# Performance work log

Measured on AMD Instinct MI355X. Metric: run time of the kernel, lower is better.

The kernel has to match this reference:

```python
import jax, jax.numpy as jnp
import numpy as np
import math

B, N, D = 2, 2048, 1024
H = 16
HD = D // H
WINDOW = 256
LN_EPS = 1e-5
NEG_INF = float('-inf')


def _alibi_slopes(num_heads):
    # num_heads=16 is a power of two -> no extra-slope branch
    closest = 2 ** math.floor(math.log2(num_heads))
    base = 2.0 ** (-(2.0 ** (-(math.log2(closest) - 3))))
    return np.power(base, np.arange(1, closest + 1, dtype=np.float32))


def setup_inputs() -> dict:
    key = jax.random.key(0)
    ks = jax.random.split(key, 8)
    s = 0.02
    return {
        'x': jax.random.normal(ks[0], (B, N, D), dtype=jnp.float32),
        'qkv_w': jax.random.normal(ks[1], (D, 3 * D), dtype=jnp.float32) * s,
        'qkv_b': jnp.zeros((3 * D,), jnp.float32),
        'proj_w': jax.random.normal(ks[2], (D, D), dtype=jnp.float32) * s,
        'proj_b': jnp.zeros((D,), jnp.float32),
        'ln1_g': jnp.ones((D,), jnp.float32),
        'ln1_b': jnp.zeros((D,), jnp.float32),
        'ln2_g': jnp.ones((D,), jnp.float32),
        'ln2_b': jnp.zeros((D,), jnp.float32),
        'fc1_w': jax.random.normal(ks[3], (D, 4 * D), dtype=jnp.float32) * s,
        'fc1_b': jnp.zeros((4 * D,), jnp.float32),
        'fc2_w': jax.random.normal(ks[4], (4 * D, D), dtype=jnp.float32) * s,
        'fc2_b': jnp.zeros((D,), jnp.float32),
    }


def _layernorm(x, g, b):
    mu = jnp.mean(x, axis=-1, keepdims=True)
    var = jnp.mean(jnp.square(x - mu), axis=-1, keepdims=True)
    return (x - mu) * jax.lax.rsqrt(var + LN_EPS) * g + b


def reference(x, qkv_w, qkv_b, proj_w, proj_b, ln1_g, ln1_b, ln2_g, ln2_b,
              fc1_w, fc1_b, fc2_w, fc2_b):
    # ---- ALiBi sliding-window causal attention (pre-norm) ----
    h = _layernorm(x, ln1_g, ln1_b)
    qkv = (h @ qkv_w + qkv_b).reshape(B, N, 3, H, HD)
    q, k, v = [jnp.transpose(qkv[:, :, i], (0, 2, 1, 3)) for i in range(3)]  # [B,H,N,HD]

    scale = HD ** -0.5
    attn = jnp.einsum('bhqd,bhkd->bhqk', q, k) * scale  # [B,H,N,N]

    pos = jnp.arange(N)
    rel = pos[None, :] - pos[:, None]                      # rel[i,j] = j - i
    slopes = jnp.asarray(_alibi_slopes(H))                 # [H]
    a = slopes[:, None, None] * jnp.abs(rel).astype(jnp.float32)
    alibi = jnp.where(rel < 0, -a, a)                      # == slopes * rel
    attn = attn + alibi[None]

    # sliding-window mask: +1.0 inside window (faithful to ones-init), -inf outside
    sw = jnp.where(jnp.abs(rel) >= WINDOW, NEG_INF, 1.0)
    attn = attn + sw[None, None]

    # causal mask
    attn = jnp.where((rel > 0)[None, None], NEG_INF, attn)

    p = jax.nn.softmax(attn, axis=-1)
    o = jnp.einsum('bhqk,bhkd->bhqd', p, v)
    o = jnp.transpose(o, (0, 2, 1, 3)).reshape(B, N, D)
    x = x + (o @ proj_w + proj_b)

    # ---- FFN (Linear -> exact GELU -> Linear), pre-norm residual ----
    h2 = _layernorm(x, ln2_g, ln2_b)
    ff = jax.nn.gelu(h2 @ fc1_w + fc1_b, approximate=False) @ fc2_w + fc2_b
    return x + ff
```

## Files before the change

kernel.cpp:

```cpp
#include <hip/hip_runtime.h>
#include <stdint.h>

typedef unsigned short u16;
typedef __attribute__((ext_vector_type(8))) short bf16x8;
typedef __attribute__((ext_vector_type(4))) float f32x4;

__device__ __forceinline__ u16 f2bf(float f) {
  union { float f; unsigned u; } x; x.f = f;
  unsigned r = x.u + 0x7fffu + ((x.u >> 16) & 1u);
  return (u16)(r >> 16);
}

__device__ __forceinline__ float gelu_fast(float v) {
  float y = 0.7978845608f * (v + 0.044715f * v * v * v);
  float e = __expf(2.0f * y);
  float th = 1.0f - 2.0f / (e + 1.0f);
  return 0.5f * v * (1.0f + th);
}

#define GLOAD16(g, l) __builtin_amdgcn_global_load_lds( \
    (const __attribute__((address_space(1))) unsigned int*)(g), \
    (__attribute__((address_space(3))) unsigned int*)(l), 16, 0, 0)

__global__ __launch_bounds__(256) void pre_kernel(
    const float* __restrict__ qkv_w, const float* __restrict__ proj_w,
    const float* __restrict__ fc1_w, const float* __restrict__ fc2_w,
    u16* __restrict__ qkvw_t, u16* __restrict__ projw_t,
    u16* __restrict__ fc1w_t, u16* __restrict__ fc2w_t,
    const float* __restrict__ x, const float* __restrict__ g,
    const float* __restrict__ be, u16* __restrict__ h1) {
  __shared__ float tile[32][33];
  __shared__ float p1[4], p2[4];
  const int bid = blockIdx.x, t = threadIdx.x;
  if (bid < 12288) {
    const float* W; u16* Wt; int K, N, base, nb;
    if (bid < 3072)      { W = qkv_w;  Wt = qkvw_t;  K = 1024; N = 3072; base = 0;    nb = 96; }
    else if (bid < 4096) { W = proj_w; Wt = projw_t; K = 1024; N = 1024; base = 3072; nb = 32; }
    else if (bid < 8192) { W = fc1_w;  Wt = fc1w_t;  K = 1024; N = 4096; base = 4096; nb = 128; }
    else                 { W = fc2_w;  Wt = fc2w_t;  K = 4096; N = 1024; base = 8192; nb = 32; }
    int r = bid - base;
    int n0 = (r % nb) * 32, k0 = (r / nb) * 32;
    int tx = t & 31, ty = t >> 5;
#pragma unroll
    for (int i = 0; i < 32; i += 8)
      tile[ty + i][tx] = W[(size_t)(k0 + ty + i) * N + n0 + tx];
    __syncthreads();
#pragma unroll
    for (int i = 0; i < 32; i += 8)
      Wt[(size_t)(n0 + ty + i) * K + k0 + tx] = f2bf(tile[tx][ty + i]);
  } else {
    int row = bid - 12288;
    const float4 v = ((const float4*)(x + (size_t)row * 1024))[t];
    float s = v.x + v.y + v.z + v.w;
#pragma unroll
    for (int m = 1; m < 64; m <<= 1) s += __shfl_xor(s, m);
    int wid = t >> 6, lane = t & 63;
    if (lane == 0) p1[wid] = s;
    __syncthreads();
    float mean = (p1[0] + p1[1] + p1[2] + p1[3]) * (1.f / 1024.f);
    float a0 = v.x - mean, a1 = v.y - mean, a2 = v.z - mean, a3 = v.w - mean;
    float ss = a0 * a0 + a1 * a1 + a2 * a2 + a3 * a3;
#pragma unroll
    for (int m = 1; m < 64; m <<= 1) ss += __shfl_xor(ss, m);
    if (lane == 0) p2[wid] = ss;
    __syncthreads();
    float var = (p2[0] + p2[1] + p2[2] + p2[3]) * (1.f / 1024.f);
    float rs = rsqrtf(var + 1e-5f);
    const float4 gg = ((const float4*)g)[t];
    const float4 bb = ((const float4*)be)[t];
    ushort4 ov;
    ov.x = f2bf(a0 * rs * gg.x + bb.x);
    ov.y = f2bf(a1 * rs * gg.y + bb.y);
    ov.z = f2bf(a2 * rs * gg.z + bb.z);
    ov.w = f2bf(a3 * rs * gg.w + bb.w);
    *(ushort4*)(h1 + (size_t)row * 1024 + t * 4) = ov;
  }
}

__global__ __launch_bounds__(256) void ln_kernel(const float* __restrict__ x,
                                                 const float* __restrict__ g,
                                                 const float* __restrict__ be,
                                                 u16* __restrict__ out) {
  int row = blockIdx.x, t = threadIdx.x;
  const float4 v = ((const float4*)(x + (size_t)row * 1024))[t];
  float s = v.x + v.y + v.z + v.w;
#pragma unroll
  for (int m = 1; m < 64; m <<= 1) s += __shfl_xor(s, m);
  __shared__ float p1[4], p2[4];
  int wid = t >> 6, lane = t & 63;
  if (lane == 0) p1[wid] = s;
  __syncthreads();
  float mean = (p1[0] + p1[1] + p1[2] + p1[3]) * (1.f / 1024.f);
  float a0 = v.x - mean, a1 = v.y - mean, a2 = v.z - mean, a3 = v.w - mean;
  float ss = a0 * a0 + a1 * a1 + a2 * a2 + a3 * a3;
#pragma unroll
  for (int m = 1; m < 64; m <<= 1) ss += __shfl_xor(ss, m);
  if (lane == 0) p2[wid] = ss;
  __syncthreads();
  float var = (p2[0] + p2[1] + p2[2] + p2[3]) * (1.f / 1024.f);
  float rs = rsqrtf(var + 1e-5f);
  const float4 gg = ((const float4*)g)[t];
  const float4 bb = ((const float4*)be)[t];
  ushort4 ov;
  ov.x = f2bf(a0 * rs * gg.x + bb.x);
  ov.y = f2bf(a1 * rs * gg.y + bb.y);
  ov.z = f2bf(a2 * rs * gg.z + bb.z);
  ov.w = f2bf(a3 * rs * gg.w + bb.w);
  *(ushort4*)(out + (size_t)row * 1024 + t * 4) = ov;
}

template <int GELU_F, int HAS_RES, int OUT_F32, int OUT_BF16>
__global__ __launch_bounds__(256) void gemm97_kernel(
    const u16* __restrict__ A, const u16* __restrict__ Bt,
    const float* __restrict__ bias, const float* __restrict__ res,
    float* __restrict__ outf, u16* __restrict__ outb, int M, int N, int K, int nbn) {
  __shared__ u16 lA[128 * 64];
  __shared__ u16 lB[128 * 64];
  const int t = threadIdx.x, lane = t & 63, wid = t >> 6;
  const int wr = wid >> 1, wc = wid & 1;
  const int nwg = gridDim.x;
  const int q = nwg >> 3, rm = nwg & 7;
  const int xcd = blockIdx.x & 7, oin = blockIdx.x >> 3;
  const int swz = (xcd < rm ? xcd * (q + 1) : rm * (q + 1) + (xcd - rm) * q) + oin;
  const int bm = swz / nbn, bn = swz % nbn;
  f32x4 acc[4][4] = {};
  const int nkt = K >> 6;

  for (int kt = 0; kt < nkt; ++kt) {
#pragma unroll
    for (int r = 0; r < 4; ++r) {
      int f = (r * 256 + t) * 16;
      int fs = f ^ (((f >> 7) & 7) << 4);
      int row = fs >> 7;
      int kb = (fs & 127) >> 1;
      GLOAD16(A + (size_t)(bm * 128 + row) * K + kt * 64 + kb, ((char*)lA) + f);
      GLOAD16(Bt + (size_t)(bn * 128 + row) * K + kt * 64 + kb, ((char*)lB) + f);
    }
    __syncthreads();
#pragma unroll
    for (int kk = 0; kk < 2; ++kk) {
      bf16x8 af[4], bfr[4];
#pragma unroll
      for (int fm = 0; fm < 4; ++fm) {
        int row = wr * 64 + fm * 16 + (lane & 15);
        int k = kk * 32 + (lane >> 4) * 8;
        af[fm] = *(const bf16x8*)((const char*)lA + ((row * 128 + k * 2) ^ ((row & 7) << 4)));
      }
#pragma unroll
      for (int fn = 0; fn < 4; ++fn) {
        int row = wc * 64 + fn * 16 + (lane & 15);
        int k = kk * 32 + (lane >> 4) * 8;
        bfr[fn] = *(const bf16x8*)((const char*)lB + ((row * 128 + k * 2) ^ ((row & 7) << 4)));
      }
#pragma unroll
      for (int fm = 0; fm < 4; ++fm)
#pragma unroll
        for (int fn = 0; fn < 4; ++fn)
          acc[fm][fn] = __builtin_amdgcn_mfma_f32_16x16x32_bf16(af[fm], bfr[fn], acc[fm][fn], 0, 0, 0);
    }
    __syncthreads();
  }

#pragma unroll
  for (int fm = 0; fm < 4; ++fm) {
#pragma unroll
    for (int fn = 0; fn < 4; ++fn) {
      int col = bn * 128 + wc * 64 + fn * 16 + (lane & 15);
      float bcol = bias[col];
#pragma unroll
      for (int r = 0; r < 4; ++r) {
        int row = bm * 128 + wr * 64 + fm * 16 + (lane >> 4) * 4 + r;
        float v = acc[fm][fn][r] + bcol;
        if constexpr (GELU_F) v = gelu_fast(v);
        size_t idx = (size_t)row * N + col;
        if constexpr (HAS_RES) v += res[idx];
        if constexpr (OUT_F32) outf[idx] = v;
        if constexpr (OUT_BF16) outb[idx] = f2bf(v);
      }
    }
  }
}

template <int BN, int GELU_F, int HAS_RES, int OUT_F32, int OUT_BF16>
__global__ __launch_bounds__(256) void gemm_kernel(
    const u16* __restrict__ A, const u16* __restrict__ Bt,
    const float* __restrict__ bias, const float* __restrict__ res,
    float* __restrict__ outf, u16* __restrict__ outb, int M, int N, int K) {
  __shared__ u16 lA[2][128 * 64];
  __shared__ u16 lB[2][BN * 64];
  const int t = threadIdx.x, lane = t & 63, wid = t >> 6;
  const int bm = blockIdx.x, bn = blockIdx.y;
  constexpr int FM = (BN == 128) ? 4 : 2;
  constexpr int FN = (BN == 128) ? 4 : (BN / 16);
  const int wr = (BN == 128) ? (wid >> 1) : wid;
  const int wc = (BN == 128) ? (wid & 1) : 0;
  f32x4 acc[FM][FN] = {};

  const int nkt = K >> 6;

  auto stage = [&](int buf, int kt) {
#pragma unroll
    for (int r = 0; r < 4; ++r) {
      int f = (r * 256 + t) * 16;
      int fs = f ^ (((f >> 7) & 7) << 4);
      int row = fs >> 7;
      int kb = (fs & 127) >> 1;
      GLOAD16(A + (size_t)(bm * 128 + row) * K + kt * 64 + kb,
              ((char*)&lA[buf][0]) + f);
    }
#pragma unroll
    for (int r = 0; r < BN / 32; ++r) {
      int f = (r * 256 + t) * 16;
      int fs = f ^ (((f >> 7) & 7) << 4);
      int row = fs >> 7;
      int kb = (fs & 127) >> 1;
      GLOAD16(Bt + (size_t)(bn * BN + row) * K + kt * 64 + kb,
              ((char*)&lB[buf][0]) + f);
    }
  };

  stage(0, 0);
  __syncthreads();

  for (int kt = 0; kt < nkt; ++kt) {
    const int cur = kt & 1;
    if (kt + 1 < nkt) stage(cur ^ 1, kt + 1);
#pragma unroll
    for (int kk = 0; kk < 2; ++kk) {
      bf16x8 af[FM], bfr[FN];
#pragma unroll
      for (int fm = 0; fm < FM; ++fm) {
        int row = wr * (FM * 16) + fm * 16 + (lane & 15);
        int k = kk * 32 + (lane >> 4) * 8;
        af[fm] = *(const bf16x8*)((const char*)&lA[cur][0] + ((row * 128 + k * 2) ^ ((row & 7) << 4)));
      }
#pragma unroll
      for (int fn = 0; fn < FN; ++fn) {
        int row = wc * 64 + fn * 16 + (lane & 15);
        int k = kk * 32 + (lane >> 4) * 8;
        bfr[fn] = *(const bf16x8*)((const char*)&lB[cur][0] + ((row * 128 + k * 2) ^ ((row & 7) << 4)));
      }
#pragma unroll
      for (int fm = 0; fm < FM; ++fm)
#pragma unroll
        for (int fn = 0; fn < FN; ++fn)
          acc[fm][fn] = __builtin_amdgcn_mfma_f32_16x16x32_bf16(af[fm], bfr[fn], acc[fm][fn], 0, 0, 0);
    }
    __syncthreads();
  }

#pragma unroll
  for (int fm = 0; fm < FM; ++fm) {
#pragma unroll
    for (int fn = 0; fn < FN; ++fn) {
      int col = bn * BN + wc * 64 + fn * 16 + (lane & 15);
      float bcol = bias[col];
#pragma unroll
      for (int r = 0; r < 4; ++r) {
        int row = bm * 128 + wr * (FM * 16) + fm * 16 + (lane >> 4) * 4 + r;
        float v = acc[fm][fn][r] + bcol;
        if constexpr (GELU_F) v = gelu_fast(v);
        size_t idx = (size_t)row * N + col;
        if constexpr (HAS_RES) v += res[idx];
        if constexpr (OUT_F32) outf[idx] = v;
        if constexpr (OUT_BF16) outb[idx] = f2bf(v);
      }
    }
  }
}

__global__ __launch_bounds__(256) void attn_kernel(const u16* __restrict__ qkv,
                                                   u16* __restrict__ o) {
  __shared__ u16 kvbuf[22016];
  __shared__ u16 lP[4][16 * 296];
  u16* lK = kvbuf;
  u16* lV = kvbuf;
  const int t = threadIdx.x, lane = t & 63, w = t >> 6;
  const int qtile = blockIdx.x, bh = blockIdx.y, b = bh >> 4, h = bh & 15;
  const int kbase = qtile * 64 - 256;
  const size_t bq = (size_t)b * 2048 * 3072;
  const float NEGBIG = -1e30f;

  for (int r = 0; r < 10; ++r) {
    int jl = r * 32 + (t >> 3);
    int d0 = (t & 7) * 8;
    int jg = kbase + jl;
    uint4 kv;
    if (jg >= 0 && jg < 2048)
      kv = *(const uint4*)(qkv + bq + (size_t)jg * 3072 + 1024 + h * 64 + d0);
    else
      kv = make_uint4(0, 0, 0, 0);
    *(uint4*)((char*)lK + ((jl * 128 + d0 * 2) ^ ((jl & 7) << 4))) = kv;
  }
  __syncthreads();

  const int i0 = qtile * 64 + w * 16;
  const int q15 = lane & 15, grp = lane >> 4;
  const u16* qrow = qkv + bq + (size_t)(i0 + q15) * 3072 + h * 64;
  bf16x8 qf0 = *(const bf16x8*)(qrow + grp * 8);
  bf16x8 qf1 = *(const bf16x8*)(qrow + 32 + grp * 8);

  f32x4 st[17];
#pragma unroll
  for (int tt = 0; tt < 17; ++tt) {
    st[tt] = f32x4{0.f, 0.f, 0.f, 0.f};
    int klb = w * 16 + tt * 16;
#pragma unroll
    for (int kk = 0; kk < 2; ++kk) {
      int row = klb + q15;
      int k = kk * 32 + grp * 8;
      bf16x8 kf = *(const bf16x8*)((const char*)lK + ((row * 128 + k * 2) ^ ((row & 7) << 4)));
      st[tt] = __builtin_amdgcn_mfma_f32_16x16x32_bf16(kf, (kk ? qf1 : qf0), st[tt], 0, 0, 0);
    }
  }

  const float slope = exp2f(-0.5f * (float)(h + 1));
  const int qg = i0 + q15;
  float mx = NEGBIG;
#pragma unroll
  for (int tt = 0; tt < 17; ++tt) {
    int kb = kbase + w * 16 + tt * 16;
#pragma unroll
    for (int r = 0; r < 4; ++r) {
      int key = kb + grp * 4 + r;
      float s = st[tt][r] * 0.125f + slope * (float)(key - qg);
      bool valid = (key >= 0) && (key <= qg) && (qg - key < 256);
      s = valid ? s : NEGBIG;
      st[tt][r] = s;
      mx = fmaxf(mx, s);
    }
  }
  mx = fmaxf(mx, __shfl_xor(mx, 16));
  mx = fmaxf(mx, __shfl_xor(mx, 32));
  float sum = 0.f;
#pragma unroll
  for (int tt = 0; tt < 17; ++tt)
#pragma unroll
    for (int r = 0; r < 4; ++r) {
      float p = __expf(st[tt][r] - mx);
      st[tt][r] = p;
      sum += p;
    }
  sum += __shfl_xor(sum, 16);
  sum += __shfl_xor(sum, 32);
  const float inv = 1.0f / sum;

  u16* Pw = &lP[w][0];
#pragma unroll
  for (int tt = 0; tt < 17; ++tt) {
    unsigned u0 = ((unsigned)f2bf(st[tt][1]) << 16) | f2bf(st[tt][0]);
    unsigned u1 = ((unsigned)f2bf(st[tt][3]) << 16) | f2bf(st[tt][2]);
    uint2 uu; uu.x = u0; uu.y = u1;
    *(uint2*)(Pw + q15 * 296 + tt * 16 + grp * 4) = uu;
  }
  { uint2 z; z.x = 0; z.y = 0; *(uint2*)(Pw + q15 * 296 + 272 + grp * 4) = z; }

  __syncthreads();

  for (int r = 0; r < 11; ++r) {
    int jl = r * 32 + (t >> 3);
    int d0 = (t & 7) * 8;
    int jg = kbase + jl;
    if (jl < 336) {
      uint4 vv;
      if (jg >= 0 && jg < 2048)
        vv = *(const uint4*)(qkv + bq + (size_t)jg * 3072 + 2048 + h * 64 + d0);
      else
        vv = make_uint4(0, 0, 0, 0);
      const u16* vs = (const u16*)&vv;
#pragma unroll
      for (int u = 0; u < 8; ++u) lV[(d0 + u) * 344 + jl] = vs[u];
    }
  }
  __syncthreads();

  f32x4 ot[4] = {};
#pragma unroll
  for (int c = 0; c < 9; ++c) {
    bf16x8 pf = *(const bf16x8*)(Pw + q15 * 296 + c * 32 + grp * 8);
#pragma unroll
    for (int hb = 0; hb < 4; ++hb) {
      bf16x8 vf = *(const bf16x8*)(lV + (hb * 16 + q15) * 344 + w * 16 + c * 32 + grp * 8);
      ot[hb] = __builtin_amdgcn_mfma_f32_16x16x32_bf16(vf, pf, ot[hb], 0, 0, 0);
    }
  }

#pragma unroll
  for (int hb = 0; hb < 4; ++hb) {
    ushort4 ov;
    ov.x = f2bf(ot[hb][0] * inv);
    ov.y = f2bf(ot[hb][1] * inv);
    ov.z = f2bf(ot[hb][2] * inv);
    ov.w = f2bf(ot[hb][3] * inv);
    *(ushort4*)(o + (size_t)(b * 2048 + i0 + q15) * 1024 + h * 64 + hb * 16 + grp * 4) = ov;
  }
}

extern "C" void kernel_launch(void* const* d_in, const int* in_sizes, int n_in,
                              void* d_out, int out_size, void* d_ws, size_t ws_size,
                              hipStream_t stream) {
  const float* x      = (const float*)d_in[0];
  const float* qkv_w  = (const float*)d_in[1];
  const float* qkv_b  = (const float*)d_in[2];
  const float* proj_w = (const float*)d_in[3];
  const float* proj_b = (const float*)d_in[4];
  const float* ln1_g  = (const float*)d_in[5];
  const float* ln1_b  = (const float*)d_in[6];
  const float* ln2_g  = (const float*)d_in[7];
  const float* ln2_b  = (const float*)d_in[8];
  const float* fc1_w  = (const float*)d_in[9];
  const float* fc1_b  = (const float*)d_in[10];
  const float* fc2_w  = (const float*)d_in[11];
  const float* fc2_b  = (const float*)d_in[12];
  float* out = (float*)d_out;

  char* ws = (char*)d_ws;
  u16* qkvw_t  = (u16*)(ws);
  u16* projw_t = (u16*)(ws + 6291456);
  u16* fc1w_t  = (u16*)(ws + 8388608);
  u16* fc2w_t  = (u16*)(ws + 16777216);
  char* BIG    = ws + 25165824;
  char* SMALL  = ws + 58720256;
  u16* qkvb = (u16*)BIG;
  u16* ff1  = (u16*)BIG;
  u16* h1   = (u16*)SMALL;
  u16* obuf = (u16*)SMALL;
  u16* h2   = (u16*)SMALL;
  float* x1 = out;

  pre_kernel<<<16384, 256, 0, stream>>>(qkv_w, proj_w, fc1_w, fc2_w,
                                        qkvw_t, projw_t, fc1w_t, fc2w_t,
                                        x, ln1_g, ln1_b, h1);
  gemm97_kernel<0, 0, 0, 1><<<768, 256, 0, stream>>>(h1, qkvw_t, qkv_b, nullptr, nullptr, qkvb, 4096, 3072, 1024, 24);
  attn_kernel<<<dim3(32, 32), 256, 0, stream>>>(qkvb, obuf);
  gemm_kernel<32, 0, 1, 1, 0><<<dim3(32, 32), 256, 0, stream>>>(obuf, projw_t, proj_b, x, x1, nullptr, 4096, 1024, 1024);
  ln_kernel<<<4096, 256, 0, stream>>>(x1, ln2_g, ln2_b, h2);
  gemm97_kernel<1, 0, 0, 1><<<1024, 256, 0, stream>>>(h2, fc1w_t, fc1_b, nullptr, nullptr, ff1, 4096, 4096, 1024, 32);
  gemm_kernel<32, 0, 1, 1, 0><<<dim3(32, 32), 256, 0, stream>>>(ff1, fc2w_t, fc2_b, x1, out, nullptr, 4096, 1024, 4096);
}
```

Before: 339.3 us.

## Enlarge QKV/FC1 GEMM tiles to 256x128 and widen proj/FC2 tiles to BN=64

Replaces the 128x128 GEMM used for the QKV and FC1 projections with a 256x128 tile in which each wave computes 128x64 and streams A fragments one at a time. This halves the block count and raises the arithmetic intensity per LDS load. The proj and FC2 GEMMs switch from BN=32 to BN=64 tiles, halving their grids. The cost is more registers and LDS per block, fewer blocks (384/512 on 256 CUs, which can leave tail imbalance), and a launch bound of 2 blocks per CU.

```diff
diff --git a/kernel.cpp b/kernel.cpp
--- a/kernel.cpp
+++ b/kernel.cpp
@@ -109,73 +109,74 @@
   *(ushort4*)(out + (size_t)row * 1024 + t * 4) = ov;
 }
 
-template <int GELU_F, int HAS_RES, int OUT_F32, int OUT_BF16>
-__global__ __launch_bounds__(256) void gemm97_kernel(
+template <int GELU_F>
+__global__ __launch_bounds__(256, 2) void gemmw_kernel(
     const u16* __restrict__ A, const u16* __restrict__ Bt,
-    const float* __restrict__ bias, const float* __restrict__ res,
-    float* __restrict__ outf, u16* __restrict__ outb, int M, int N, int K, int nbn) {
-  __shared__ u16 lA[128 * 64];
+    const float* __restrict__ bias, u16* __restrict__ outb,
+    int M, int N, int K, int nbn) {
+  __shared__ u16 lA[256 * 64];
   __shared__ u16 lB[128 * 64];
   const int t = threadIdx.x, lane = t & 63, wid = t >> 6;
-  const int wr = wid >> 1, wc = wid & 1;
+  const int wm = wid >> 1, wn = wid & 1;
+  const int q15 = lane & 15, grp = lane >> 4;
   const int nwg = gridDim.x;
-  const int q = nwg >> 3, rm = nwg & 7;
+  const int qq = nwg >> 3, rm = nwg & 7;
   const int xcd = blockIdx.x & 7, oin = blockIdx.x >> 3;
-  const int swz = (xcd < rm ? xcd * (q + 1) : rm * (q + 1) + (xcd - rm) * q) + oin;
+  const int swz = (xcd < rm ? xcd * (qq + 1) : rm * (qq + 1) + (xcd - rm) * qq) + oin;
   const int bm = swz / nbn, bn = swz % nbn;
-  f32x4 acc[4][4] = {};
+
+  f32x4 acc[8][4] = {};
   const int nkt = K >> 6;
 
   for (int kt = 0; kt < nkt; ++kt) {
+#pragma unroll
+    for (int r = 0; r < 8; ++r) {
+      int f = (r * 256 + t) * 16;
+      int fs = f ^ (((f >> 7) & 7) << 4);
+      int row = fs >> 7, kb = (fs & 127) >> 1;
+      GLOAD16(A + (size_t)(bm * 256 + row) * K + kt * 64 + kb, ((char*)lA) + f);
+    }
 #pragma unroll
     for (int r = 0; r < 4; ++r) {
       int f = (r * 256 + t) * 16;
       int fs = f ^ (((f >> 7) & 7) << 4);
-      int row = fs >> 7;
-      int kb = (fs & 127) >> 1;
-      GLOAD16(A + (size_t)(bm * 128 + row) * K + kt * 64 + kb, ((char*)lA) + f);
+      int row = fs >> 7, kb = (fs & 127) >> 1;
       GLOAD16(Bt + (size_t)(bn * 128 + row) * K + kt * 64 + kb, ((char*)lB) + f);
     }
     __syncthreads();
 #pragma unroll
     for (int kk = 0; kk < 2; ++kk) {
-      bf16x8 af[4], bfr[4];
-#pragma unroll
-      for (int fm = 0; fm < 4; ++fm) {
-        int row = wr * 64 + fm * 16 + (lane & 15);
-        int k = kk * 32 + (lane >> 4) * 8;
-        af[fm] = *(const bf16x8*)((const char*)lA + ((row * 128 + k * 2) ^ ((row & 7) << 4)));
-      }
+      const int k = kk * 32 + grp * 8;
+      bf16x8 bfr[4];
 #pragma unroll
       for (int fn = 0; fn < 4; ++fn) {
-        int row = wc * 64 + fn * 16 + (lane & 15);
-        int k = kk * 32 + (lane >> 4) * 8;
+        int row = wn * 64 + fn * 16 + q15;
         bfr[fn] = *(const bf16x8*)((const char*)lB + ((row * 128 + k * 2) ^ ((row & 7) << 4)));
       }
 #pragma unroll
-      for (int fm = 0; fm < 4; ++fm)
+      for (int j = 0; j < 8; ++j) {
+        int row = wm * 128 + j * 16 + q15;
+        bf16x8 af = *(const bf16x8*)((const char*)lA + ((row * 128 + k * 2) ^ ((row & 7) << 4)));
 #pragma unroll
         for (int fn = 0; fn < 4; ++fn)
-          acc[fm][fn] = __builtin_amdgcn_mfma_f32_16x16x32_bf16(af[fm], bfr[fn], acc[fm][fn], 0, 0, 0);
-    }
-    __syncthreads();
-  }
-
-#pragma unroll
-  for (int fm = 0; fm < 4; ++fm) {
+          acc[j][fn] = __builtin_amdgcn_mfma_f32_16x16x32_bf16(af, bfr[fn], acc[j][fn], 0, 0, 0);
+      }
+    }
+    __syncthreads();
+  }
+
+#pragma unroll
+  for (int j = 0; j < 8; ++j) {
 #pragma unroll
     for (int fn = 0; fn < 4; ++fn) {
-      int col = bn * 128 + wc * 64 + fn * 16 + (lane & 15);
+      int col = bn * 128 + wn * 64 + fn * 16 + q15;
       float bcol = bias[col];
 #pragma unroll
       for (int r = 0; r < 4; ++r) {
-        int row = bm * 128 + wr * 64 + fm * 16 + (lane >> 4) * 4 + r;
-        float v = acc[fm][fn][r] + bcol;
+        int row = bm * 256 + wm * 128 + j * 16 + grp * 4 + r;
+        float v = acc[j][fn][r] + bcol;
         if constexpr (GELU_F) v = gelu_fast(v);
-        size_t idx = (size_t)row * N + col;
-        if constexpr (HAS_RES) v += res[idx];
-        if constexpr (OUT_F32) outf[idx] = v;
-        if constexpr (OUT_BF16) outb[idx] = f2bf(v);
+        outb[(size_t)row * N + col] = f2bf(v);
       }
     }
   }
@@ -431,10 +432,10 @@
   pre_kernel<<<16384, 256, 0, stream>>>(qkv_w, proj_w, fc1_w, fc2_w,
                                         qkvw_t, projw_t, fc1w_t, fc2w_t,
                                         x, ln1_g, ln1_b, h1);
-  gemm97_kernel<0, 0, 0, 1><<<768, 256, 0, stream>>>(h1, qkvw_t, qkv_b, nullptr, nullptr, qkvb, 4096, 3072, 1024, 24);
+  gemmw_kernel<0><<<384, 256, 0, stream>>>(h1, qkvw_t, qkv_b, qkvb, 4096, 3072, 1024, 24);
   attn_kernel<<<dim3(32, 32), 256, 0, stream>>>(qkvb, obuf);
-  gemm_kernel<32, 0, 1, 1, 0><<<dim3(32, 32), 256, 0, stream>>>(obuf, projw_t, proj_b, x, x1, nullptr, 4096, 1024, 1024);
+  gemm_kernel<64, 0, 1, 1, 0><<<dim3(32, 16), 256, 0, stream>>>(obuf, projw_t, proj_b, x, x1, nullptr, 4096, 1024, 1024);
   ln_kernel<<<4096, 256, 0, stream>>>(x1, ln2_g, ln2_b, h2);
-  gemm97_kernel<1, 0, 0, 1><<<1024, 256, 0, stream>>>(h2, fc1w_t, fc1_b, nullptr, nullptr, ff1, 4096, 4096, 1024, 32);
-  gemm_kernel<32, 0, 1, 1, 0><<<dim3(32, 32), 256, 0, stream>>>(ff1, fc2w_t, fc2_b, x1, out, nullptr, 4096, 1024, 4096);
-}
+  gemmw_kernel<1><<<512, 256, 0, stream>>>(h2, fc1w_t, fc1_b, ff1, 4096, 4096, 1024, 32);
+  gemm_kernel<64, 0, 1, 1, 0><<<dim3(32, 16), 256, 0, stream>>>(ff1, fc2w_t, fc2_b, x1, out, nullptr, 4096, 1024, 4096);
+}
```

Result: faster. 313.7 us (-7.5%).
